# Kernel tuning notes

Hardware: AMD Instinct MI355X
Metric: run time of the kernel (lower is better)

Reference implementation:

```python
import jax, jax.numpy as jnp
import numpy as np
from math import factorial

IRREPS_IN1 = [(128, 0), (64, 1), (32, 2)]  # (mul, l): features
IRREPS_IN2 = [(1, 0), (1, 1), (1, 2)]      # spherical harmonics lmax=2
BATCH = 16384

# ---------- real Clebsch-Gordan coefficients (e3nn convention) ----------

def _su2_cg(j1, j2, j3, m1, m2, m3):
    if m3 != m1 + m2:
        return 0.0
    f = factorial
    pref = ((2 * j3 + 1) * f(j1 + j2 - j3) * f(j1 - j2 + j3) * f(-j1 + j2 + j3) / f(j1 + j2 + j3 + 1)) ** 0.5
    pref *= (f(j3 + m3) * f(j3 - m3) * f(j1 - m1) * f(j1 + m1) * f(j2 - m2) * f(j2 + m2)) ** 0.5
    s = 0.0
    for v in range(0, j1 + j2 - j3 + 1):
        a = j1 + j2 - j3 - v; b = j1 - m1 - v; c = j2 + m2 - v
        d = j3 - j2 + m1 + v; e = j3 - j1 - m2 + v
        if min(a, b, c, d, e) < 0:
            continue
        s += (-1) ** v / (f(v) * f(a) * f(b) * f(c) * f(d) * f(e))
    return pref * s


def _su2_cg_tensor(l1, l2, l3):
    C = np.zeros((2 * l1 + 1, 2 * l2 + 1, 2 * l3 + 1))
    for m1 in range(-l1, l1 + 1):
        for m2 in range(-l2, l2 + 1):
            for m3 in range(-l3, l3 + 1):
                C[l1 + m1, l2 + m2, l3 + m3] = _su2_cg(l1, l2, l3, m1, m2, m3)
    return C


def _q(l):
    # change of basis real -> complex spherical harmonics
    q = np.zeros((2 * l + 1, 2 * l + 1), dtype=np.complex128)
    for m in range(-l, 0):
        q[l + m, l + abs(m)] = 1.0 / np.sqrt(2.0)
        q[l + m, l - abs(m)] = -1j / np.sqrt(2.0)
    q[l, l] = 1.0
    for m in range(1, l + 1):
        q[l + m, l + abs(m)] = (-1) ** m / np.sqrt(2.0)
        q[l + m, l - abs(m)] = 1j * (-1) ** m / np.sqrt(2.0)
    return (-1j) ** l * q


def _real_cg(l1, l2, l3):
    C = _su2_cg_tensor(l1, l2, l3).astype(np.complex128)
    Q1, Q2, Q3 = _q(l1), _q(l2), _q(l3)
    C = np.einsum('ij,kl,mn,ikn->jlm', Q1, Q2, np.conj(Q3.T), C)
    assert np.abs(C.imag).max() < 1e-8
    return np.ascontiguousarray(C.real.astype(np.float32))

# precompute all CG tensors needed by the full tensor product
CG = {}
for _m1, _l1 in IRREPS_IN1:
    for _m2, _l2 in IRREPS_IN2:
        for _l3 in range(abs(_l1 - _l2), _l1 + _l2 + 1):
            if (_l1, _l2, _l3) not in CG:
                CG[(_l1, _l2, _l3)] = _real_cg(_l1, _l2, _l3)


def _tensor_product(x, y):
    """Full CG tensor product. x:[B,480] y:[B,9] -> dict l3 -> list of [B,mul,2l3+1]."""
    B = x.shape[0]
    outs = {}
    off1 = 0
    for mul1, l1 in IRREPS_IN1:
        d1 = 2 * l1 + 1
        x_blk = x[:, off1:off1 + mul1 * d1].reshape(B, mul1, d1)
        off1 += mul1 * d1
        off2 = 0
        for mul2, l2 in IRREPS_IN2:
            d2 = 2 * l2 + 1
            y_blk = y[:, off2:off2 + mul2 * d2].reshape(B, mul2, d2)
            off2 += mul2 * d2
            for l3 in range(abs(l1 - l2), l1 + l2 + 1):
                cg = jnp.asarray(CG[(l1, l2, l3)])  # [d1,d2,d3]
                z = jnp.einsum('ijk,bui,bvj->buvk', cg, x_blk, y_blk)
                outs.setdefault(l3, []).append(z.reshape(B, mul1 * mul2, 2 * l3 + 1))
    return outs


def setup_inputs() -> dict:
    key = jax.random.key(0)
    k = jax.random.split(key, 5)
    dim1 = sum(m * (2 * l + 1) for m, l in IRREPS_IN1)  # 480
    dim2 = sum(m * (2 * l + 1) for m, l in IRREPS_IN2)  # 9
    x = jax.random.normal(k[0], (BATCH, dim1), dtype=jnp.float32)
    y = jax.random.normal(k[1], (BATCH, dim2), dtype=jnp.float32)
    # fan-in per output l of the equivariant Linear (tp outputs with matching l)
    W0 = jax.random.normal(k[2], (224, 128), dtype=jnp.float32)
    W1 = jax.random.normal(k[3], (384, 64), dtype=jnp.float32)
    W2 = jax.random.normal(k[4], (352, 32), dtype=jnp.float32)
    return {"x": x, "y": y, "W0": W0, "W1": W1, "W2": W2}


def reference(x, y, W0, W1, W2):
    B = x.shape[0]
    outs = _tensor_product(x, y)
    Ws = {0: W0, 1: W1, 2: W2}
    res = []
    for mul_out, l in IRREPS_IN1:
        blk = jnp.concatenate(outs[l], axis=1)  # [B, tot_mul, 2l+1]
        tot_mul = blk.shape[1]
        o = jnp.einsum('bui,uv->bvi', blk, Ws[l]) / np.sqrt(tot_mul).astype(np.float32)
        res.append(o.reshape(B, mul_out * (2 * l + 1)))
    return jnp.concatenate(res, axis=1)  # [B, 480]
```

## Files before the change

### kernel.cpp

```cpp
#include <hip/hip_runtime.h>
#include <math.h>
#include <stdint.h>

#define NBATCH 16384
#define MB 16
#define NT 256
#define NBLOCKS (NBATCH/MB)
#define WT_BYTE_OFF 2560

typedef float  f32x4 __attribute__((ext_vector_type(4)));
typedef short  s16x8 __attribute__((ext_vector_type(8)));

constexpr double cfact(int n){ double r=1.0; for(int i=2;i<=n;++i) r*=(double)i; return r; }
constexpr double csqrt_(double x){
  if (x<=0.0) return 0.0;
  double m=x, k=1.0;
  while (m>1.0) { m*=0.25; k*=2.0; }
  while (m<0.25){ m*=4.0;  k*=0.5; }
  double g=0.7;
  for(int i=0;i<14;++i) g = 0.5*(g + m/g);
  return g*k;
}
constexpr double su2d(int j1,int j2,int j3,int m1,int m2,int m3){
  if (m1+m2 != m3) return 0.0;
  double pref = csqrt_((double)(2*j3+1)*cfact(j1+j2-j3)*cfact(j1-j2+j3)*cfact(-j1+j2+j3)/cfact(j1+j2+j3+1));
  pref *= csqrt_(cfact(j3+m3)*cfact(j3-m3)*cfact(j1-m1)*cfact(j1+m1)*cfact(j2-m2)*cfact(j2+m2));
  double s=0.0;
  for (int v=0; v<=j1+j2-j3; ++v){
    int a=j1+j2-j3-v, b=j1-m1-v, c=j2+m2-v, d=j3-j2+m1+v, e=j3-j1-m2+v;
    if (a<0||b<0||c<0||d<0||e<0) continue;
    double t = 1.0/(cfact(v)*cfact(a)*cfact(b)*cfact(c)*cfact(d)*cfact(e));
    s += (v&1)? -t : t;
  }
  return pref*s;
}
struct C2 { double re, im; };
constexpr C2 qvald(int l,int r,int c){
  int m = r - l;
  const double is2 = 0.70710678118654752440;
  double br=0.0, bi=0.0;
  if (m<0){ if (c==l-m) br=is2; else if (c==l+m) bi=-is2; }
  else if (m==0){ if (c==l) br=1.0; }
  else { double sg=(m&1)?-1.0:1.0; if (c==l+m) br=sg*is2; else if (c==l-m) bi=sg*is2; }
  if (l==1){ double nr=bi, ni=-br; br=nr; bi=ni; }
  else if (l==2){ br=-br; bi=-bi; }
  return C2{br,bi};
}
constexpr int HP_L1[15]={0,1,2,0,1,1,1,2,2,0,1,1,2,2,2};
constexpr int HP_L2[15]={0,1,2,1,0,1,2,1,2,2,1,2,0,1,2};
constexpr int HP_L3[15]={0,0,0,1,1,1,1,1,1,2,2,2,2,2,2};
constexpr int HP_CGOFF[15]={0,1,10,35,44,53,80,125,170,245,270,315,390,415,490};
constexpr int HP_TSTART[15]={0,1,4,9,12,21,30,39,54,69,74,89,104,129,154};
constexpr int HP_YOFF[15]={0,1,4,1,0,1,4,1,4,4,1,4,0,1,4};

struct CGT { float v[616]; };
constexpr CGT make_cg_part(int p0, int p1){
  CGT T{};
  for (int z=0; z<616; ++z) T.v[z]=0.f;
  for (int p=p0; p<p1; ++p){
    int l1=HP_L1[p], l2=HP_L2[p], l3=HP_L3[p];
    int d1=2*l1+1, d2=2*l2+1, d3=2*l3+1;
    double su[5][5]={};
    for (int i=0;i<d1;++i) for (int k=0;k<d2;++k){
      int n = i+k-l1-l2+l3;
      su[i][k] = (n>=0 && n<d3) ? su2d(l1,l2,l3, i-l1, k-l2, n-l3) : 0.0;
    }
    for (int i1=0;i1<d1;++i1) for (int i2=0;i2<d2;++i2) for (int i3=0;i3<d3;++i3){
      double val=0.0;
      for (int i=0;i<d1;++i) for (int k=0;k<d2;++k){
        int n = i+k-l1-l2+l3;
        if (n<0||n>=d3) continue;
        double c = su[i][k];
        if (c==0.0) continue;
        C2 q1=qvald(l1,i,i1), q2=qvald(l2,k,i2), q3=qvald(l3,n,i3);
        double ar = q1.re*q2.re - q1.im*q2.im;
        double ai = q1.re*q2.im + q1.im*q2.re;
        val += (ar*q3.re + ai*q3.im)*c;
      }
      T.v[HP_CGOFF[p] + (i1*d2+i2)*d3 + i3] = (float)val;
    }
  }
  return T;
}
constexpr CGT CG_A = make_cg_part(0,8);
constexpr CGT CG_B = make_cg_part(8,12);
constexpr CGT CG_D = make_cg_part(12,15);
constexpr CGT cg_merge(){
  CGT T{};
  for (int i=0;i<616;++i) T.v[i] = CG_A.v[i] + CG_B.v[i] + CG_D.v[i];
  return T;
}
__device__ __constant__ const CGT CGC = cg_merge();

constexpr uint32_t make_td(int e){
  if (e>=179) return 0u;
  int p=0; while (p<14 && e>=HP_TSTART[p+1]) ++p;
  int r = e - HP_TSTART[p];
  int d2 = 2*HP_L2[p]+1, d3 = 2*HP_L3[p]+1;
  int i1 = r/d3, j3 = r - (r/d3)*d3;
  int base = HP_CGOFF[p] + i1*d2*d3 + j3;
  return (uint32_t)base | ((uint32_t)d2<<10) | ((uint32_t)d3<<13) | ((uint32_t)HP_YOFF[p]<<16);
}
struct TDT { uint32_t v[192]; };
constexpr TDT make_tdt(){ TDT t{}; for(int e=0;e<192;++e) t.v[e]=make_td(e); return t; }
__device__ __constant__ const TDT TDC = make_tdt();

constexpr uint16_t cmap1(int o){
  if (o<128) return (uint16_t)o;
  if (o<320){ int s=o-128; int i1=s>>6; int u=s&63; return (uint16_t)(128 + u*3 + i1); }
  if (o<480){ int s=o-320; int i1=s>>5; int u=s&31; return (uint16_t)(320 + u*5 + i1); }
  return (uint16_t)0xFFFF;
}
struct CMT { uint16_t v[512]; };
constexpr CMT make_cm(){ CMT t{}; for(int o=0;o<512;++o) t.v[o]=cmap1(o); return t; }
__device__ __constant__ const CMT CMC = make_cm();

__device__ const int   SEG_WB[15] = {0,16384,24576, 28672,36864,40960,45056,49152,51200,
                                     53248,57344,59392,61440,62464,63488};
__device__ const int   SEG_SH[15] = {7,6,5, 7,6,6,6,5,5, 7,6,6,5,5,5};
__device__ const int   SEG_U0[15] = {0,128,192, 0,128,192,256,320,352, 0,128,192,256,288,320};
__device__ const int   SEG_G[15]  = {0,0,0, 1,1,1,1,1,1, 2,2,2,2,2,2};
__device__ const float SEG_SC[3]  = {0.066815310478f, 0.051031036308f, 0.053300179089f};

__device__ __forceinline__ uint32_t f2bf(float f){
  uint32_t u = __float_as_uint(f);
  return (u + 0x7fffu + ((u>>16)&1u)) >> 16;
}
__device__ __forceinline__ float bf2f(uint32_t v){ return __uint_as_float(v << 16); }

__global__ __launch_bounds__(NT) void prep(const float* __restrict__ x, const float* __restrict__ y,
                     const float* __restrict__ W0, const float* __restrict__ W1,
                     const float* __restrict__ W2, float* __restrict__ ws, float* __restrict__ out)
{
  const int blk = blockIdx.x, tid = threadIdx.x;
  if (blk >= 1024){
    int t = (blk-1024)*NT + tid;
    uint16_t* wt = (uint16_t*)((char*)ws + WT_BYTE_OFF);
    int j = 0;
    while (j < 14 && t >= SEG_WB[j+1]) ++j;
    int idx = t - SEG_WB[j];
    int sh = SEG_SH[j];
    int v  = idx >> sh, u1 = idx & ((1<<sh)-1);
    int g  = SEG_G[j];
    int N  = (g==0)?128:(g==1)?64:32;
    const float* Wsrc = (g==0)?W0:(g==1)?W1:W2;
    wt[t] = (uint16_t)f2bf(Wsrc[(SEG_U0[j]+u1)*N + v] * SEG_SC[g]);
    return;
  }

  __shared__ __align__(16) float    xs[MB*480];
  __shared__ __align__(16) float    ysm[MB*9];
  __shared__ __align__(16) uint16_t cml[512];

  const int b0 = blk*MB;
  {
    const float4* src = (const float4*)(x + (size_t)b0*480);
    float4* dst = (float4*)xs;
    #pragma unroll
    for (int it = 0; it < 8; ++it){
      int i = it*NT + tid;
      if (i < 1920) dst[i] = src[i];
    }
  }
  if (tid < 144) ysm[tid] = y[(size_t)b0*9 + tid];
  if (tid < 128) ((uint4*)cml)[tid & 63] = ((const uint4*)CMC.v)[tid & 63];
  __syncthreads();

  char* obase = (char*)out + (size_t)blk*30720;

  #pragma unroll
  for (int it = 0; it < 4; ++it){
    const int chunk = it*NT + tid;
    const int b = chunk >> 6, c16 = chunk & 63;
    uint16_t vals[8];
    #pragma unroll
    for (int jj = 0; jj < 8; ++jj){
      const uint16_t c = cml[c16*8 + jj];
      const float v = (c == 0xFFFFu) ? 0.f : xs[b*480 + c];
      vals[jj] = (uint16_t)f2bf(v);
    }
    *(uint4*)(obase + b*1024 + ((c16*16) ^ ((b&7)<<4))) = *(const uint4*)vals;
  }

  if (tid < 179){
    const uint32_t td = TDC.v[tid];
    const int base = td & 1023, d2 = (td>>10)&7, str = (td>>13)&7, yoff = (td>>16)&7;
    uint16_t tv[16];
    #pragma unroll
    for (int b = 0; b < 16; ++b){
      float t = 0.f;
      for (int i2 = 0; i2 < d2; ++i2) t += CGC.v[base + i2*str] * ysm[b*9 + yoff + i2];
      tv[b] = (uint16_t)f2bf(t);
    }
    char* dst = obase + 16384 + tid*32;
    *(uint4*)dst      = *(const uint4*)&tv[0];
    *(uint4*)(dst+16) = *(const uint4*)&tv[8];
  }
}

template<int G> struct GM;
template<> struct GM<0>{
  static constexpr int NS=3, D3=1, NMT=2, NI3=1;
  static constexpr int MUL[3]={128,64,32};
  static constexpr int D1[3] ={1,3,5};
  static constexpr int XB[3] ={0,128,320};
  static constexpr int TS[3] ={0,1,4};
  static constexpr int WB[3] ={0,16384,24576};
};
template<> struct GM<1>{
  static constexpr int NS=6, D3=3, NMT=1, NI3=3;
  static constexpr int MUL[6]={128,64,64,64,32,32};
  static constexpr int D1[6] ={1,3,3,3,5,5};
  static constexpr int XB[6] ={0,128,128,128,320,320};
  static constexpr int TS[6] ={9,12,21,30,39,54};
  static constexpr int WB[6] ={28672,36864,40960,45056,49152,51200};
};
template<> struct GM<2>{
  static constexpr int NS=6, D3=5, NMT=1, NI3=3;
  static constexpr int MUL[6]={128,64,64,32,32,32};
  static constexpr int D1[6] ={1,3,3,5,5,5};
  static constexpr int XB[6] ={0,128,128,320,320,320};
  static constexpr int TS[6] ={69,74,89,104,129,154};
  static constexpr int WB[6] ={53248,57344,59392,61440,62464,63488};
};

template<int G, int S, int NMT, int NI3>
__device__ __forceinline__ void do_seg(const short* __restrict__ wt,
                                       const uint16_t* __restrict__ xp,
                                       const uint16_t* __restrict__ Tsh,
                                       f32x4 (&acc)[NMT][NI3],
                                       int ln, int koct, int mt0, int i3base, int ni3)
{
  using M = GM<G>;
  constexpr int MUL = M::MUL[S];
  constexpr int KS  = MUL >> 5;
  constexpr int D1  = M::D1[S];

  s16x8 Af[NMT][KS];
  #pragma unroll
  for (int mt = 0; mt < NMT; ++mt)
    #pragma unroll
    for (int kk = 0; kk < KS; ++kk)
      Af[mt][kk] = *(const s16x8*)(wt + M::WB[S] + ((mt0+mt)*16 + ln)*MUL + kk*32 + koct);

  const int swz = (ln & 7) << 4;
  const int koct2 = koct*2;
  const char* xrow = (const char*)xp + ln*1024;

  #pragma unroll
  for (int i1 = 0; i1 < D1; ++i1){
    s16x8 Bf[KS];
    #pragma unroll
    for (int kk = 0; kk < KS; ++kk){
      const int cb = (M::XB[S] + i1*MUL + kk*32)*2 + koct2;
      Bf[kk] = *(const s16x8*)(xrow + (cb ^ swz));
    }
    f32x4 D[NMT];
    #pragma unroll
    for (int mt = 0; mt < NMT; ++mt){
      D[mt] = (f32x4){0.f,0.f,0.f,0.f};
      #pragma unroll
      for (int kk = 0; kk < KS; ++kk)
        D[mt] = __builtin_amdgcn_mfma_f32_16x16x32_bf16(Af[mt][kk], Bf[kk], D[mt], 0, 0, 0);
    }
    #pragma unroll
    for (int j = 0; j < NI3; ++j){
      if (j < ni3){
        const int e = M::TS[S] + i1*M::D3 + i3base + j;
        const float tv = bf2f(Tsh[e*16 + ln]);
        #pragma unroll
        for (int mt = 0; mt < NMT; ++mt){
          acc[mt][j][0] += tv*D[mt][0];
          acc[mt][j][1] += tv*D[mt][1];
          acc[mt][j][2] += tv*D[mt][2];
          acc[mt][j][3] += tv*D[mt][3];
        }
      }
    }
  }
}

template<int G>
__device__ __forceinline__ void run_group(const short* __restrict__ wt,
                                          float* __restrict__ out, int b0, int tid,
                                          const uint16_t* __restrict__ Tsh,
                                          const uint16_t* __restrict__ xp)
{
  using M = GM<G>;
  const int lane = tid & 63, w = tid >> 6;
  const int ln   = lane & 15;
  const int koct = (lane >> 4) * 8;
  constexpr int NMT = M::NMT, NI3 = M::NI3;

  int mt0, i3base, ni3;
  if constexpr (G == 0){ mt0 = 2*w; i3base = 0; ni3 = 1; }
  else if constexpr (G == 1){ mt0 = w; i3base = 0; ni3 = 3; }
  else { mt0 = w >> 1; i3base = (w & 1)*3; ni3 = (w & 1) ? 2 : 3; }

  f32x4 acc[NMT][NI3];
  #pragma unroll
  for (int a = 0; a < NMT; ++a)
    #pragma unroll
    for (int b = 0; b < NI3; ++b) acc[a][b] = (f32x4){0.f,0.f,0.f,0.f};

  do_seg<G,0,NMT,NI3>(wt, xp, Tsh, acc, ln, koct, mt0, i3base, ni3);
  do_seg<G,1,NMT,NI3>(wt, xp, Tsh, acc, ln, koct, mt0, i3base, ni3);
  do_seg<G,2,NMT,NI3>(wt, xp, Tsh, acc, ln, koct, mt0, i3base, ni3);
  if constexpr (M::NS > 3){
    do_seg<G,(M::NS>3)?3:0,NMT,NI3>(wt, xp, Tsh, acc, ln, koct, mt0, i3base, ni3);
    do_seg<G,(M::NS>4)?4:0,NMT,NI3>(wt, xp, Tsh, acc, ln, koct, mt0, i3base, ni3);
    do_seg<G,(M::NS>5)?5:0,NMT,NI3>(wt, xp, Tsh, acc, ln, koct, mt0, i3base, ni3);
  }

  const int rq = (lane >> 4) * 4;
  float* orow = out + (size_t)(b0 + ln)*480;
  if constexpr (G == 0){
    #pragma unroll
    for (int mt = 0; mt < NMT; ++mt){
      const int vb = (mt0+mt)*16 + rq;
      float4 st = make_float4(acc[mt][0][0], acc[mt][0][1], acc[mt][0][2], acc[mt][0][3]);
      *(float4*)(orow + vb) = st;
    }
  } else if constexpr (G == 1){
    const int vb = mt0*16 + rq;
    float buf[12];
    #pragma unroll
    for (int r = 0; r < 4; ++r)
      #pragma unroll
      for (int j = 0; j < 3; ++j) buf[r*3+j] = acc[0][j][r];
    float* p = orow + 128 + vb*3;
    *(float4*)(p)   = make_float4(buf[0],buf[1],buf[2],buf[3]);
    *(float4*)(p+4) = make_float4(buf[4],buf[5],buf[6],buf[7]);
    *(float4*)(p+8) = make_float4(buf[8],buf[9],buf[10],buf[11]);
  } else {
    const int vb = mt0*16 + rq;
    #pragma unroll
    for (int r = 0; r < 4; ++r)
      #pragma unroll
      for (int j = 0; j < 3; ++j)
        if (j < ni3)
          orow[320 + (vb+r)*5 + i3base + j] = acc[0][j][r];
  }
}

__global__ __launch_bounds__(NT) void tp_linear(const float* __restrict__ ws,
                                                float* __restrict__ out)
{
  __shared__ __align__(16) uint16_t xp[MB*512];
  __shared__ __align__(16) uint16_t Tsh[192*16];
  const int tid = threadIdx.x;
  const int b0 = blockIdx.x * MB;
  const short* wt = (const short*)((const char*)ws + WT_BYTE_OFF);
  const char* blkbase = (const char*)out + (size_t)blockIdx.x*30720;
  const int wv = tid >> 6, l64 = tid & 63;

  #pragma unroll
  for (int off = 0; off < 16384; off += 4096){
    const int a = off + wv*1024 + l64*16;
    *(uint4*)((char*)xp + a) = *(const uint4*)(blkbase + a);
  }
  {
    const int a = wv*1024 + l64*16;
    *(uint4*)((char*)Tsh + a) = *(const uint4*)(blkbase + 16384 + a);
  }
  if (wv < 2){
    const int a = 4096 + wv*1024 + l64*16;
    *(uint4*)((char*)Tsh + a) = *(const uint4*)(blkbase + 16384 + a);
  }
  __syncthreads();

  run_group<0>(wt, out, b0, tid, Tsh, xp);
  run_group<1>(wt, out, b0, tid, Tsh, xp);
  run_group<2>(wt, out, b0, tid, Tsh, xp);
}

extern "C" void kernel_launch(void* const* d_in, const int* in_sizes, int n_in,
                              void* d_out, int out_size, void* d_ws, size_t ws_size,
                              hipStream_t stream)
{
  const float* x  = (const float*)d_in[0];
  const float* y  = (const float*)d_in[1];
  const float* W0 = (const float*)d_in[2];
  const float* W1 = (const float*)d_in[3];
  const float* W2 = (const float*)d_in[4];
  float* out = (float*)d_out;
  float* ws  = (float*)d_ws;

  hipLaunchKernelGGL(prep, dim3(1276), dim3(NT), 0, stream, x, y, W0, W1, W2, ws, out);
  hipLaunchKernelGGL(tp_linear, dim3(NBLOCKS), dim3(NT), 0, stream, ws, out);
}
```

Measured before the change: 128.9 us.

## Fuse x/y packing into the tensor-product kernel, keep weight packing separate

Moves the per-block bf16 packing of x and the CG-times-y table into the main tensor-product kernel, building them in shared memory instead of staging them through the output buffer in global memory. A small separate kernel now only packs the weights. This removes a global round trip for the staged operands and the prep work that shared the first launch. In exchange the main kernel uses more shared memory (an extra bf16 copy of x), which may lower occupancy, and packing now sits on its critical path before the matrix work.

```diff
diff --git a/kernel.cpp b/kernel.cpp
--- a/kernel.cpp
+++ b/kernel.cpp
@@ -128,74 +128,20 @@
 }
 __device__ __forceinline__ float bf2f(uint32_t v){ return __uint_as_float(v << 16); }
 
-__global__ __launch_bounds__(NT) void prep(const float* __restrict__ x, const float* __restrict__ y,
-                     const float* __restrict__ W0, const float* __restrict__ W1,
-                     const float* __restrict__ W2, float* __restrict__ ws, float* __restrict__ out)
-{
-  const int blk = blockIdx.x, tid = threadIdx.x;
-  if (blk >= 1024){
-    int t = (blk-1024)*NT + tid;
-    uint16_t* wt = (uint16_t*)((char*)ws + WT_BYTE_OFF);
-    int j = 0;
-    while (j < 14 && t >= SEG_WB[j+1]) ++j;
-    int idx = t - SEG_WB[j];
-    int sh = SEG_SH[j];
-    int v  = idx >> sh, u1 = idx & ((1<<sh)-1);
-    int g  = SEG_G[j];
-    int N  = (g==0)?128:(g==1)?64:32;
-    const float* Wsrc = (g==0)?W0:(g==1)?W1:W2;
-    wt[t] = (uint16_t)f2bf(Wsrc[(SEG_U0[j]+u1)*N + v] * SEG_SC[g]);
-    return;
-  }
-
-  __shared__ __align__(16) float    xs[MB*480];
-  __shared__ __align__(16) float    ysm[MB*9];
-  __shared__ __align__(16) uint16_t cml[512];
-
-  const int b0 = blk*MB;
-  {
-    const float4* src = (const float4*)(x + (size_t)b0*480);
-    float4* dst = (float4*)xs;
-    #pragma unroll
-    for (int it = 0; it < 8; ++it){
-      int i = it*NT + tid;
-      if (i < 1920) dst[i] = src[i];
-    }
-  }
-  if (tid < 144) ysm[tid] = y[(size_t)b0*9 + tid];
-  if (tid < 128) ((uint4*)cml)[tid & 63] = ((const uint4*)CMC.v)[tid & 63];
-  __syncthreads();
-
-  char* obase = (char*)out + (size_t)blk*30720;
-
-  #pragma unroll
-  for (int it = 0; it < 4; ++it){
-    const int chunk = it*NT + tid;
-    const int b = chunk >> 6, c16 = chunk & 63;
-    uint16_t vals[8];
-    #pragma unroll
-    for (int jj = 0; jj < 8; ++jj){
-      const uint16_t c = cml[c16*8 + jj];
-      const float v = (c == 0xFFFFu) ? 0.f : xs[b*480 + c];
-      vals[jj] = (uint16_t)f2bf(v);
-    }
-    *(uint4*)(obase + b*1024 + ((c16*16) ^ ((b&7)<<4))) = *(const uint4*)vals;
-  }
-
-  if (tid < 179){
-    const uint32_t td = TDC.v[tid];
-    const int base = td & 1023, d2 = (td>>10)&7, str = (td>>13)&7, yoff = (td>>16)&7;
-    uint16_t tv[16];
-    #pragma unroll
-    for (int b = 0; b < 16; ++b){
-      float t = 0.f;
-      for (int i2 = 0; i2 < d2; ++i2) t += CGC.v[base + i2*str] * ysm[b*9 + yoff + i2];
-      tv[b] = (uint16_t)f2bf(t);
-    }
-    char* dst = obase + 16384 + tid*32;
-    *(uint4*)dst      = *(const uint4*)&tv[0];
-    *(uint4*)(dst+16) = *(const uint4*)&tv[8];
-  }
+__global__ __launch_bounds__(NT) void pack_w(const float* __restrict__ W0, const float* __restrict__ W1,
+                                             const float* __restrict__ W2, float* __restrict__ ws)
+{
+  int t = blockIdx.x*NT + threadIdx.x;
+  uint16_t* wt = (uint16_t*)((char*)ws + WT_BYTE_OFF);
+  int j = 0;
+  while (j < 14 && t >= SEG_WB[j+1]) ++j;
+  int idx = t - SEG_WB[j];
+  int sh = SEG_SH[j];
+  int v  = idx >> sh, u1 = idx & ((1<<sh)-1);
+  int g  = SEG_G[j];
+  int N  = (g==0)?128:(g==1)?64:32;
+  const float* Wsrc = (g==0)?W0:(g==1)?W1:W2;
+  wt[t] = (uint16_t)f2bf(Wsrc[(SEG_U0[j]+u1)*N + v] * SEG_SC[g]);
 }
 
 template<int G> struct GM;
@@ -343,29 +289,62 @@
   }
 }
 
-__global__ __launch_bounds__(NT) void tp_linear(const float* __restrict__ ws,
-                                                float* __restrict__ out)
-{
+__global__ __launch_bounds__(NT) void tp_fused(const float* __restrict__ x,
+                                               const float* __restrict__ y,
+                                               const float* __restrict__ ws,
+                                               float* __restrict__ out)
+{
+  __shared__ __align__(16) uint16_t xs[MB*480];
   __shared__ __align__(16) uint16_t xp[MB*512];
   __shared__ __align__(16) uint16_t Tsh[192*16];
+  __shared__ __align__(16) float    ysm[MB*9];
+  __shared__ __align__(16) uint16_t cml[512];
+
   const int tid = threadIdx.x;
   const int b0 = blockIdx.x * MB;
   const short* wt = (const short*)((const char*)ws + WT_BYTE_OFF);
-  const char* blkbase = (const char*)out + (size_t)blockIdx.x*30720;
-  const int wv = tid >> 6, l64 = tid & 63;
+
+  {
+    const float4* src = (const float4*)(x + (size_t)b0*480);
+    #pragma unroll
+    for (int it = 0; it < 8; ++it){
+      int i = it*NT + tid;
+      if (i < 1920){
+        float4 v = src[i];
+        uint16_t p[4] = {(uint16_t)f2bf(v.x),(uint16_t)f2bf(v.y),
+                         (uint16_t)f2bf(v.z),(uint16_t)f2bf(v.w)};
+        *(uint2*)(&xs[i*4]) = *(const uint2*)p;
+      }
+    }
+  }
+  if (tid < 144) ysm[tid] = y[(size_t)b0*9 + tid];
+  else if (tid >= 192) ((uint4*)cml)[tid-192] = ((const uint4*)CMC.v)[tid-192];
+  __syncthreads();
 
   #pragma unroll
-  for (int off = 0; off < 16384; off += 4096){
-    const int a = off + wv*1024 + l64*16;
-    *(uint4*)((char*)xp + a) = *(const uint4*)(blkbase + a);
-  }
-  {
-    const int a = wv*1024 + l64*16;
-    *(uint4*)((char*)Tsh + a) = *(const uint4*)(blkbase + 16384 + a);
-  }
-  if (wv < 2){
-    const int a = 4096 + wv*1024 + l64*16;
-    *(uint4*)((char*)Tsh + a) = *(const uint4*)(blkbase + 16384 + a);
+  for (int it = 0; it < 4; ++it){
+    const int chunk = it*NT + tid;
+    const int b = chunk >> 6, c16 = chunk & 63;
+    uint16_t vals[8];
+    #pragma unroll
+    for (int jj = 0; jj < 8; ++jj){
+      const uint16_t c = cml[c16*8 + jj];
+      vals[jj] = (c == 0xFFFFu) ? (uint16_t)0 : xs[b*480 + c];
+    }
+    *(uint4*)((char*)xp + b*1024 + ((c16*16) ^ ((b&7)<<4))) = *(const uint4*)vals;
+  }
+  if (tid < 179){
+    const uint32_t td = TDC.v[tid];
+    const int base = td & 1023, d2 = (td>>10)&7, str = (td>>13)&7, yoff = (td>>16)&7;
+    uint16_t tv[16];
+    #pragma unroll
+    for (int b = 0; b < 16; ++b){
+      float t = 0.f;
+      for (int i2 = 0; i2 < d2; ++i2) t += CGC.v[base + i2*str] * ysm[b*9 + yoff + i2];
+      tv[b] = (uint16_t)f2bf(t);
+    }
+    *(uint4*)(&Tsh[tid*16])     = *(const uint4*)&tv[0];
+    *(uint4*)(&Tsh[tid*16 + 8]) = *(const uint4*)&tv[8];
   }
   __syncthreads();
 
@@ -386,6 +365,6 @@
   float* out = (float*)d_out;
   float* ws  = (float*)d_ws;
 
-  hipLaunchKernelGGL(prep, dim3(1276), dim3(NT), 0, stream, x, y, W0, W1, W2, ws, out);
-  hipLaunchKernelGGL(tp_linear, dim3(NBLOCKS), dim3(NT), 0, stream, ws, out);
-}
+  hipLaunchKernelGGL(pack_w, dim3(252), dim3(NT), 0, stream, W0, W1, W2, ws);
+  hipLaunchKernelGGL(tp_fused, dim3(NBLOCKS), dim3(NT), 0, stream, x, y, ws, out);
+}
```

Result: no change. 127.7 us (-0.9%).
